# Kernel optimization log

Measured on AMD Instinct MI355X. Metric: run time of the kernel, lower is better.

The kernel has to match this reference:

```python
import jax, jax.numpy as jnp
import numpy as np

M, N, D, P = 1024, 1024, 64, 4096
H = N // D
L = P + M  # total KV length


def setup_inputs() -> dict:
    key = jax.random.key(0)
    ks = jax.random.split(key, 7)
    s = 1.0 / np.float32(np.sqrt(N))
    return {
        "X": jax.random.normal(ks[0], (M, N), jnp.float32),
        "W_q": jax.random.normal(ks[1], (N, N), jnp.float32) * s,
        "W_k": jax.random.normal(ks[2], (N, N), jnp.float32) * s,
        "W_v": jax.random.normal(ks[3], (N, N), jnp.float32) * s,
        "cache_K": jax.random.normal(ks[4], (H, P, D), jnp.float32),
        "cache_V": jax.random.normal(ks[5], (H, P, D), jnp.float32),
        "noise": jax.random.normal(ks[6], (H, M, L), jnp.float32) * 0.5,
    }


def reference(X, W_q, W_k, W_v, cache_K, cache_V, noise):
    # Projections: [M, N] -> [M, H, D]
    q = (X @ W_q).reshape(M, H, D)
    k = (X @ W_k).reshape(M, H, D).transpose(1, 0, 2)  # [H, M, D]
    v = (X @ W_v).reshape(M, H, D).transpose(1, 0, 2)  # [H, M, D]

    # KV cache concat (HND layout): [H, L, D]
    k_cache = jnp.concatenate([cache_K, k], axis=1)
    v_cache = jnp.concatenate([cache_V, v], axis=1)

    # Full QK^T scores, sm_scale=1.0, non-causal (flashinfer default): [H, M, L]
    scores = jnp.einsum("mhd,hld->hml", q, k_cache)
    weights = jax.nn.softmax(scores, axis=-1)  # == flash-attention probs (sm_scale=1.0)

    # Attention output: [M, H, D] -> [M, N]
    output = jnp.einsum("hml,hld->mhd", weights, v_cache).reshape(M, N)

    # Keyformer noise-perturbed importance softmax (temperature 1.5): [H, M, L]
    perturb_out = jax.nn.softmax((scores + noise) / 1.5, axis=-1)

    return output, weights, perturb_out
```

## Files before the change

kernel.cpp:

```cpp
#include <hip/hip_runtime.h>
#include <stdint.h>

#define MM 1024
#define NN 1024
#define DD 64
#define PP 4096
#define HH 16
#define LL 5120
#define SHC 12.0f

typedef float  f32x4  __attribute__((ext_vector_type(4)));
typedef short  s16x8  __attribute__((ext_vector_type(8)));
typedef short  s16x4  __attribute__((ext_vector_type(4)));
typedef __bf16 bf16x8 __attribute__((ext_vector_type(8)));

static __device__ __forceinline__ unsigned short f2bf(float f) {
    unsigned u = __float_as_uint(f);
    u += 0x7FFFu + ((u >> 16) & 1u);
    return (unsigned short)(u >> 16);
}
static __device__ __forceinline__ float bf2f(unsigned short h) {
    return __uint_as_float(((unsigned)h) << 16);
}
static __device__ __forceinline__ f32x4 mfma16(s16x8 a, s16x8 b, f32x4 c) {
    return __builtin_amdgcn_mfma_f32_16x16x32_bf16(
        __builtin_bit_cast(bf16x8, a), __builtin_bit_cast(bf16x8, b), c, 0, 0, 0);
}

__global__ void k_prep(const float* __restrict__ X, const float* __restrict__ cK,
                       unsigned short* __restrict__ Xh, unsigned short* __restrict__ Xl,
                       unsigned short* __restrict__ Kall) {
    const int nX4 = (MM * NN) / 4;
    const int nK4 = (HH * PP * DD) / 4;
    int stride = gridDim.x * blockDim.x;
    for (int i = blockIdx.x * blockDim.x + threadIdx.x; i < nX4 + nK4; i += stride) {
        if (i < nX4) {
            f32x4 v = reinterpret_cast<const f32x4*>(X)[i];
            s16x4 h, l;
            for (int j = 0; j < 4; ++j) {
                float f = v[j];
                unsigned short hb = f2bf(f);
                h[j] = (short)hb;
                l[j] = (short)f2bf(f - bf2f(hb));
            }
            reinterpret_cast<s16x4*>(Xh)[i] = h;
            reinterpret_cast<s16x4*>(Xl)[i] = l;
        } else {
            int j = i - nX4;
            f32x4 v = reinterpret_cast<const f32x4*>(cK)[j];
            s16x4 h;
            for (int jj = 0; jj < 4; ++jj) h[jj] = (short)f2bf(v[jj]);
            int e = j * 4;
            int hh = e >> 18;
            int rem = e & 262143;
            int64_t de = (int64_t)hh * (LL * DD) + rem;
            *reinterpret_cast<s16x4*>(Kall + de) = h;
        }
    }
}

__global__ void k_transW(const float* __restrict__ Wq, const float* __restrict__ Wk,
                         const float* __restrict__ Wv,
                         unsigned short* __restrict__ WhT, unsigned short* __restrict__ WlT) {
    __shared__ float t[64][68];
    int z = blockIdx.z;
    const float* W = (z == 0) ? Wq : ((z == 1) ? Wk : Wv);
    int n0 = blockIdx.x * 64, k0 = blockIdx.y * 64;
    int tc = threadIdx.x & 15, tr = threadIdx.x >> 4;
    for (int i = 0; i < 4; ++i) {
        int r = tr + i * 16;
        f32x4 v = *reinterpret_cast<const f32x4*>(W + (int64_t)(k0 + r) * NN + n0 + tc * 4);
        t[r][tc * 4 + 0] = v[0]; t[r][tc * 4 + 1] = v[1];
        t[r][tc * 4 + 2] = v[2]; t[r][tc * 4 + 3] = v[3];
    }
    __syncthreads();
    int64_t zoff = (int64_t)z * MM * NN;
    for (int i = 0; i < 4; ++i) {
        int rr = tr + i * 16;
        s16x4 h, l;
        for (int j = 0; j < 4; ++j) {
            float f = t[tc * 4 + j][rr];
            unsigned short hb = f2bf(f);
            h[j] = (short)hb;
            l[j] = (short)f2bf(f - bf2f(hb));
        }
        *reinterpret_cast<s16x4*>(WhT + zoff + (int64_t)(n0 + rr) * NN + k0 + tc * 4) = h;
        *reinterpret_cast<s16x4*>(WlT + zoff + (int64_t)(n0 + rr) * NN + k0 + tc * 4) = l;
    }
}

__launch_bounds__(256, 4)
__global__ void k_gemm(const unsigned short* __restrict__ Xh, const unsigned short* __restrict__ Xl,
                       const unsigned short* __restrict__ WhT, const unsigned short* __restrict__ WlT,
                       unsigned short* __restrict__ Qh, unsigned short* __restrict__ Ql,
                       unsigned short* __restrict__ Kall, unsigned short* __restrict__ Vproj) {
    __shared__ unsigned short sb[2 * 64 * 72];
    unsigned short* As = sb;
    unsigned short* Bs = sb + 64 * 72;
    int z = blockIdx.z;
    int n0 = blockIdx.x * 64, m0 = blockIdx.y * 64;
    int tid = threadIdx.x, lane = tid & 63, wave = tid >> 6;
    int lrow = lane & 15, lgrp = lane >> 4;
    int wm = (wave >> 1) * 32, wn = (wave & 1) * 32;
    f32x4 acc[2][2] = {};
    for (int seg = 0; seg < 3; ++seg) {
        const unsigned short* Asrc = (seg == 2) ? Xl : Xh;
        const unsigned short* Bsrc = ((seg == 1) ? WlT : WhT) + (int64_t)z * MM * NN;
        for (int kt = 0; kt < 16; ++kt) {
            int kb = kt * 64;
            for (int i = 0; i < 2; ++i) {
                int idx = i * 256 + tid;
                int r = idx >> 3, c8 = (idx & 7) * 8;
                *reinterpret_cast<s16x8*>(&As[r * 72 + c8]) =
                    *reinterpret_cast<const s16x8*>(Asrc + (int64_t)(m0 + r) * NN + kb + c8);
                *reinterpret_cast<s16x8*>(&Bs[r * 72 + c8]) =
                    *reinterpret_cast<const s16x8*>(Bsrc + (int64_t)(n0 + r) * NN + kb + c8);
            }
            __syncthreads();
            for (int ks = 0; ks < 2; ++ks) {
                s16x8 af[2], bfr[2];
                for (int f = 0; f < 2; ++f)
                    af[f] = *reinterpret_cast<const s16x8*>(&As[(wm + f * 16 + lrow) * 72 + ks * 32 + lgrp * 8]);
                for (int f = 0; f < 2; ++f)
                    bfr[f] = *reinterpret_cast<const s16x8*>(&Bs[(wn + f * 16 + lrow) * 72 + ks * 32 + lgrp * 8]);
                for (int i = 0; i < 2; ++i)
                    for (int j = 0; j < 2; ++j)
                        acc[i][j] = mfma16(af[i], bfr[j], acc[i][j]);
            }
            __syncthreads();
        }
    }
    unsigned short* Cs = sb;
    auto stageC = [&](int lo) {
        for (int i = 0; i < 2; ++i)
            for (int j = 0; j < 2; ++j)
                for (int r = 0; r < 4; ++r) {
                    float v = acc[i][j][r];
                    unsigned short hv = f2bf(v);
                    if (lo) hv = f2bf(v - bf2f(hv));
                    Cs[(wm + i * 16 + lgrp * 4 + r) * 72 + wn + j * 16 + lrow] = hv;
                }
    };
    auto writeC = [&](unsigned short* dst, int kmode) {
        for (int i = 0; i < 2; ++i) {
            int idx = i * 256 + tid;
            int r = idx >> 3, c8 = (idx & 7) * 8;
            s16x8 v = *reinterpret_cast<const s16x8*>(&Cs[r * 72 + c8]);
            int gm = m0 + r, gn = n0 + c8;
            if (kmode) {
                int hh = gn >> 6, d = gn & 63;
                *reinterpret_cast<s16x8*>(dst + ((int64_t)hh * LL + PP + gm) * DD + d) = v;
            } else {
                *reinterpret_cast<s16x8*>(dst + (int64_t)gm * NN + gn) = v;
            }
        }
    };
    __syncthreads();
    if (z == 0) {
        stageC(0); __syncthreads(); writeC(Qh, 0);
        __syncthreads(); stageC(1); __syncthreads(); writeC(Ql, 0);
    } else if (z == 1) {
        stageC(0); __syncthreads(); writeC(Kall, 1);
    } else {
        stageC(0); __syncthreads(); writeC(Vproj, 0);
    }
}

__global__ void k_transV(const float* __restrict__ cV, const unsigned short* __restrict__ Vproj,
                         unsigned short* __restrict__ VT) {
    __shared__ unsigned short Ts[64][72];
    int b = blockIdx.x;
    int hh = b / 80, lt = b % 80;
    int l0 = lt * 64;
    int tid = threadIdx.x;
    if (l0 < PP) {
        for (int i = 0; i < 4; ++i) {
            int idx = i * 256 + tid;
            int r = idx >> 4, c4 = (idx & 15) * 4;
            f32x4 v = *reinterpret_cast<const f32x4*>(cV + ((int64_t)hh * PP + l0 + r) * DD + c4);
            s16x4 o;
            for (int j = 0; j < 4; ++j) o[j] = (short)f2bf(v[j]);
            *reinterpret_cast<s16x4*>(&Ts[r][c4]) = o;
        }
    } else {
        for (int i = 0; i < 2; ++i) {
            int idx = i * 256 + tid;
            int r = idx >> 3, c8 = (idx & 7) * 8;
            *reinterpret_cast<s16x8*>(&Ts[r][c8]) =
                *reinterpret_cast<const s16x8*>(Vproj + (int64_t)(l0 - PP + r) * NN + hh * DD + c8);
        }
    }
    __syncthreads();
    for (int i = 0; i < 2; ++i) {
        int idx = i * 256 + tid;
        int d = idx >> 3, l8 = (idx & 7) * 8;
        s16x8 v;
        for (int j = 0; j < 8; ++j) v[j] = (short)Ts[l8 + j][d];
        *reinterpret_cast<s16x8*>(VT + ((int64_t)hh * DD + d) * LL + l0 + l8) = v;
    }
}

__launch_bounds__(256, 4)
__global__ void k_attn2(const unsigned short* __restrict__ Qh, const unsigned short* __restrict__ Ql,
                        const unsigned short* __restrict__ Kall, const unsigned short* __restrict__ VT,
                        const float* __restrict__ noise,
                        float* __restrict__ outO, float* __restrict__ outW, float* __restrict__ outP) {
    __shared__ __align__(16) char smem[26624];
    __shared__ float sred[4][16][2];
    __shared__ float siwp[16][2];

    int id = blockIdx.x;
    int xcd = id & 7, j = id >> 3;
    int hh = xcd * 2 + (j >> 6);
    int mt = j & 63;
    int m0 = mt * 16;
    int tid = threadIdx.x, lane = tid & 63, wave = tid >> 6;
    int lrow = lane & 15, lgrp = lane >> 4;

    float (*scf)[68] = (float(*)[68])(smem + wave * 6656);
    unsigned short (*wls)[72] = (unsigned short(*)[72])(smem + wave * 6656 + 4352);

    s16x8 aqh[2], aql[2];
    for (int ks = 0; ks < 2; ++ks) {
        int64_t off = (int64_t)(m0 + lrow) * NN + hh * DD + ks * 32 + lgrp * 8;
        aqh[ks] = *reinterpret_cast<const s16x8*>(Qh + off);
        aql[ks] = *reinterpret_cast<const s16x8*>(Ql + off);
    }
    const unsigned short* Kh = Kall + (int64_t)hh * LL * DD;
    const unsigned short* Vh = VT + (int64_t)hh * DD * LL;
    const float* nzw = noise + ((int64_t)hh * MM + m0) * LL;
    float* Wb = outW + ((int64_t)hh * MM + m0) * LL;
    float* Pb = outP + ((int64_t)hh * MM + m0) * LL;

    float SwR[4] = {}, SpR[4] = {};
    for (int c = 0; c < 20; ++c) {
        int lb = c * 256 + wave * 64;
        f32x4 nv[4];
        for (int rp = 0; rp < 4; ++rp)
            nv[rp] = *reinterpret_cast<const f32x4*>(
                nzw + (int64_t)(rp * 4 + lgrp) * LL + lb + lrow * 4);
        f32x4 sacc[4] = {};
        for (int ks = 0; ks < 2; ++ks)
            for (int lf = 0; lf < 4; ++lf) {
                s16x8 bk = *reinterpret_cast<const s16x8*>(
                    Kh + (int64_t)(lb + lf * 16 + lrow) * DD + ks * 32 + lgrp * 8);
                sacc[lf] = mfma16(aqh[ks], bk, sacc[lf]);
                sacc[lf] = mfma16(aql[ks], bk, sacc[lf]);
            }
        for (int lf = 0; lf < 4; ++lf)
            for (int r = 0; r < 4; ++r)
                scf[lgrp * 4 + r][lf * 16 + lrow] = sacc[lf][r];
        for (int rp = 0; rp < 4; ++rp) {
            f32x4 s = *reinterpret_cast<const f32x4*>(&scf[rp * 4 + lgrp][lrow * 4]);
            for (int jj = 0; jj < 4; ++jj) {
                SwR[rp] += __expf(s[jj] - SHC);
                SpR[rp] += __expf((s[jj] + nv[rp][jj]) * (1.f / 1.5f) - SHC);
            }
        }
    }
    for (int rp = 0; rp < 4; ++rp)
        for (int d = 1; d < 16; d <<= 1) {
            SwR[rp] += __shfl_xor(SwR[rp], d, 64);
            SpR[rp] += __shfl_xor(SpR[rp], d, 64);
        }
    if (lrow == 0)
        for (int rp = 0; rp < 4; ++rp) {
            sred[wave][rp * 4 + lgrp][0] = SwR[rp];
            sred[wave][rp * 4 + lgrp][1] = SpR[rp];
        }
    __syncthreads();
    if (tid < 32) {
        int row = tid >> 1, ty = tid & 1;
        float S = sred[0][row][ty] + sred[1][row][ty] + sred[2][row][ty] + sred[3][row][ty];
        siwp[row][ty] = 1.f / S;
    }
    __syncthreads();
    float iwr[4], ipr[4];
    for (int rp = 0; rp < 4; ++rp) {
        iwr[rp] = siwp[rp * 4 + lgrp][0];
        ipr[rp] = siwp[rp * 4 + lgrp][1];
    }

    f32x4 oacc[4] = {};
    for (int c = 19; c >= 0; --c) {
        int lb = c * 256 + wave * 64;
        f32x4 nv[4];
        for (int rp = 0; rp < 4; ++rp)
            nv[rp] = *reinterpret_cast<const f32x4*>(
                nzw + (int64_t)(rp * 4 + lgrp) * LL + lb + lrow * 4);
        f32x4 sacc[4] = {};
        for (int ks = 0; ks < 2; ++ks)
            for (int lf = 0; lf < 4; ++lf) {
                s16x8 bk = *reinterpret_cast<const s16x8*>(
                    Kh + (int64_t)(lb + lf * 16 + lrow) * DD + ks * 32 + lgrp * 8);
                sacc[lf] = mfma16(aqh[ks], bk, sacc[lf]);
                sacc[lf] = mfma16(aql[ks], bk, sacc[lf]);
            }
        for (int lf = 0; lf < 4; ++lf)
            for (int r = 0; r < 4; ++r)
                scf[lgrp * 4 + r][lf * 16 + lrow] = sacc[lf][r];
        for (int rp = 0; rp < 4; ++rp) {
            int row = rp * 4 + lgrp;
            f32x4 s = *reinterpret_cast<const f32x4*>(&scf[row][lrow * 4]);
            f32x4 wv, pv;
            for (int jj = 0; jj < 4; ++jj) {
                wv[jj] = __expf(s[jj] - SHC) * iwr[rp];
                pv[jj] = __expf((s[jj] + nv[rp][jj]) * (1.f / 1.5f) - SHC) * ipr[rp];
            }
            *reinterpret_cast<f32x4*>(Wb + (int64_t)row * LL + lb + lrow * 4) = wv;
            *reinterpret_cast<f32x4*>(Pb + (int64_t)row * LL + lb + lrow * 4) = pv;
            s16x4 pk;
            for (int jj = 0; jj < 4; ++jj) pk[jj] = (short)f2bf(wv[jj]);
            *reinterpret_cast<s16x4*>(&wls[row][lrow * 4]) = pk;
        }
        for (int ks = 0; ks < 2; ++ks) {
            s16x8 bw = *reinterpret_cast<const s16x8*>(&wls[lrow][ks * 32 + lgrp * 8]);
            for (int df = 0; df < 4; ++df) {
                s16x8 av = *reinterpret_cast<const s16x8*>(
                    Vh + (int64_t)(df * 16 + lrow) * LL + lb + ks * 32 + lgrp * 8);
                oacc[df] = mfma16(av, bw, oacc[df]);
            }
        }
    }
    __syncthreads();
    float* ored = (float*)smem;
    for (int df = 0; df < 4; ++df)
        for (int r = 0; r < 4; ++r)
            ored[(wave * 64 + df * 16 + lgrp * 4 + r) * 17 + lrow] = oacc[df][r];
    __syncthreads();
    for (int i = 0; i < 4; ++i) {
        int idx = i * 256 + tid;
        int m = idx >> 6, d = idx & 63;
        float v = ored[d * 17 + m] + ored[(64 + d) * 17 + m] +
                  ored[(128 + d) * 17 + m] + ored[(192 + d) * 17 + m];
        outO[(int64_t)(m0 + m) * NN + hh * DD + d] = v;
    }
}

extern "C" void kernel_launch(void* const* d_in, const int* in_sizes, int n_in,
                              void* d_out, int out_size, void* d_ws, size_t ws_size,
                              hipStream_t stream) {
    const float* X  = (const float*)d_in[0];
    const float* Wq = (const float*)d_in[1];
    const float* Wk = (const float*)d_in[2];
    const float* Wv = (const float*)d_in[3];
    const float* cK = (const float*)d_in[4];
    const float* cV = (const float*)d_in[5];
    const float* nz = (const float*)d_in[6];

    char* ws = (char*)d_ws;
    const int64_t U = 1 << 21;
    unsigned short* Xh    = (unsigned short*)(ws + 0 * U);
    unsigned short* Xl    = (unsigned short*)(ws + 1 * U);
    unsigned short* WhT   = (unsigned short*)(ws + 2 * U);
    unsigned short* WlT   = (unsigned short*)(ws + 5 * U);
    unsigned short* Qh    = (unsigned short*)(ws + 8 * U);
    unsigned short* Ql    = (unsigned short*)(ws + 9 * U);
    unsigned short* Kall  = (unsigned short*)(ws + 10 * U);
    unsigned short* Vproj = (unsigned short*)(ws + 15 * U);
    unsigned short* VT    = (unsigned short*)(ws + 16 * U);

    float* outO = (float*)d_out;
    float* outW = outO + (int64_t)MM * NN;
    float* outP = outW + (int64_t)HH * MM * LL;

    k_prep<<<2048, 256, 0, stream>>>(X, cK, Xh, Xl, Kall);
    k_transW<<<dim3(16, 16, 3), 256, 0, stream>>>(Wq, Wk, Wv, WhT, WlT);
    k_gemm<<<dim3(16, 16, 3), 256, 0, stream>>>(Xh, Xl, WhT, WlT, Qh, Ql, Kall, Vproj);
    k_transV<<<1280, 256, 0, stream>>>(cV, Vproj, VT);
    k_attn2<<<1024, 256, 0, stream>>>(Qh, Ql, Kall, VT, nz, outO, outW, outP);
}
```

Baseline: 513.6 us.

## Split attention into sum and emit kernels over KV halves with partial-output reduction

Splits the single two-pass attention kernel into a row-sum kernel and an emit kernel, each dividing the KV length into two halves, which doubles the grid to 2048 blocks. Partial softmax denominators and partial outputs go to workspace, and a small final kernel adds the two output halves. Noise is loaded per row inside the loop rather than prefetched, W/P stores become nontemporal, and the emit kernel walks blocks in reverse order, likely to reuse cached K and noise. The aim is more parallelism and occupancy. The cost is two extra launches, workspace traffic, and overwriting the Xh/WhT regions, which are no longer needed at that point.

```diff
diff --git a/kernel.cpp b/kernel.cpp
--- a/kernel.cpp
+++ b/kernel.cpp
@@ -200,25 +200,24 @@
     }
 }
 
-__launch_bounds__(256, 4)
-__global__ void k_attn2(const unsigned short* __restrict__ Qh, const unsigned short* __restrict__ Ql,
-                        const unsigned short* __restrict__ Kall, const unsigned short* __restrict__ VT,
-                        const float* __restrict__ noise,
-                        float* __restrict__ outO, float* __restrict__ outW, float* __restrict__ outP) {
-    __shared__ __align__(16) char smem[26624];
+__launch_bounds__(256, 8)
+__global__ void k_attnS(const unsigned short* __restrict__ Qh, const unsigned short* __restrict__ Ql,
+                        const unsigned short* __restrict__ Kall,
+                        const float* __restrict__ noise, float* __restrict__ wsS) {
+    __shared__ __align__(16) char smem[17408];
     __shared__ float sred[4][16][2];
-    __shared__ float siwp[16][2];
 
     int id = blockIdx.x;
-    int xcd = id & 7, j = id >> 3;
-    int hh = xcd * 2 + (j >> 6);
-    int mt = j & 63;
+    int xcd = id & 7, i = id >> 3;
+    int hh = xcd * 2 + (i >> 7);
+    int rem = i & 127;
+    int mt = rem >> 1, half = rem & 1;
     int m0 = mt * 16;
+    int w = hh * 128 + mt * 2 + half;
     int tid = threadIdx.x, lane = tid & 63, wave = tid >> 6;
     int lrow = lane & 15, lgrp = lane >> 4;
 
-    float (*scf)[68] = (float(*)[68])(smem + wave * 6656);
-    unsigned short (*wls)[72] = (unsigned short(*)[72])(smem + wave * 6656 + 4352);
+    float (*scf)[68] = (float(*)[68])(smem + wave * 4352);
 
     s16x8 aqh[2], aql[2];
     for (int ks = 0; ks < 2; ++ks) {
@@ -227,18 +226,11 @@
         aql[ks] = *reinterpret_cast<const s16x8*>(Ql + off);
     }
     const unsigned short* Kh = Kall + (int64_t)hh * LL * DD;
-    const unsigned short* Vh = VT + (int64_t)hh * DD * LL;
     const float* nzw = noise + ((int64_t)hh * MM + m0) * LL;
-    float* Wb = outW + ((int64_t)hh * MM + m0) * LL;
-    float* Pb = outP + ((int64_t)hh * MM + m0) * LL;
 
     float SwR[4] = {}, SpR[4] = {};
-    for (int c = 0; c < 20; ++c) {
-        int lb = c * 256 + wave * 64;
-        f32x4 nv[4];
-        for (int rp = 0; rp < 4; ++rp)
-            nv[rp] = *reinterpret_cast<const f32x4*>(
-                nzw + (int64_t)(rp * 4 + lgrp) * LL + lb + lrow * 4);
+    for (int c = 0; c < 10; ++c) {
+        int lb = half * 2560 + c * 256 + wave * 64;
         f32x4 sacc[4] = {};
         for (int ks = 0; ks < 2; ++ks)
             for (int lf = 0; lf < 4; ++lf) {
@@ -251,10 +243,12 @@
             for (int r = 0; r < 4; ++r)
                 scf[lgrp * 4 + r][lf * 16 + lrow] = sacc[lf][r];
         for (int rp = 0; rp < 4; ++rp) {
-            f32x4 s = *reinterpret_cast<const f32x4*>(&scf[rp * 4 + lgrp][lrow * 4]);
+            int row = rp * 4 + lgrp;
+            f32x4 s = *reinterpret_cast<const f32x4*>(&scf[row][lrow * 4]);
+            f32x4 nv = *reinterpret_cast<const f32x4*>(nzw + (int64_t)row * LL + lb + lrow * 4);
             for (int jj = 0; jj < 4; ++jj) {
                 SwR[rp] += __expf(s[jj] - SHC);
-                SpR[rp] += __expf((s[jj] + nv[rp][jj]) * (1.f / 1.5f) - SHC);
+                SpR[rp] += __expf((s[jj] + nv[jj]) * (1.f / 1.5f) - SHC);
             }
         }
     }
@@ -271,23 +265,55 @@
     __syncthreads();
     if (tid < 32) {
         int row = tid >> 1, ty = tid & 1;
-        float S = sred[0][row][ty] + sred[1][row][ty] + sred[2][row][ty] + sred[3][row][ty];
-        siwp[row][ty] = 1.f / S;
-    }
-    __syncthreads();
+        wsS[w * 32 + tid] = sred[0][row][ty] + sred[1][row][ty] +
+                            sred[2][row][ty] + sred[3][row][ty];
+    }
+}
+
+__launch_bounds__(256, 6)
+__global__ void k_attnE(const unsigned short* __restrict__ Qh, const unsigned short* __restrict__ Ql,
+                        const unsigned short* __restrict__ Kall, const unsigned short* __restrict__ VT,
+                        const float* __restrict__ noise, const float* __restrict__ wsS,
+                        float* __restrict__ wsO, float* __restrict__ outW, float* __restrict__ outP) {
+    __shared__ __align__(16) char smem[17408];
+
+    int id = blockIdx.x;
+    int xcd = id & 7, i = 255 - (id >> 3);
+    int hh = xcd * 2 + (i >> 7);
+    int rem = i & 127;
+    int mt = rem >> 1, half = rem & 1;
+    int m0 = mt * 16;
+    int w = hh * 128 + mt * 2 + half;
+    int tid = threadIdx.x, lane = tid & 63, wave = tid >> 6;
+    int lrow = lane & 15, lgrp = lane >> 4;
+
+    float (*scf)[68] = (float(*)[68])(smem + wave * 4352);
+    unsigned short* wl = (unsigned short*)scf;
+
+    s16x8 aqh[2], aql[2];
+    for (int ks = 0; ks < 2; ++ks) {
+        int64_t off = (int64_t)(m0 + lrow) * NN + hh * DD + ks * 32 + lgrp * 8;
+        aqh[ks] = *reinterpret_cast<const s16x8*>(Qh + off);
+        aql[ks] = *reinterpret_cast<const s16x8*>(Ql + off);
+    }
+    const unsigned short* Kh = Kall + (int64_t)hh * LL * DD;
+    const unsigned short* Vh = VT + (int64_t)hh * DD * LL;
+    const float* nzw = noise + ((int64_t)hh * MM + m0) * LL;
+    float* Wb = outW + ((int64_t)hh * MM + m0) * LL;
+    float* Pb = outP + ((int64_t)hh * MM + m0) * LL;
+
     float iwr[4], ipr[4];
     for (int rp = 0; rp < 4; ++rp) {
-        iwr[rp] = siwp[rp * 4 + lgrp][0];
-        ipr[rp] = siwp[rp * 4 + lgrp][1];
+        int row = rp * 4 + lgrp;
+        float sw = wsS[w * 32 + row * 2]     + wsS[(w ^ 1) * 32 + row * 2];
+        float sp = wsS[w * 32 + row * 2 + 1] + wsS[(w ^ 1) * 32 + row * 2 + 1];
+        iwr[rp] = 1.f / sw;
+        ipr[rp] = 1.f / sp;
     }
 
     f32x4 oacc[4] = {};
-    for (int c = 19; c >= 0; --c) {
-        int lb = c * 256 + wave * 64;
-        f32x4 nv[4];
-        for (int rp = 0; rp < 4; ++rp)
-            nv[rp] = *reinterpret_cast<const f32x4*>(
-                nzw + (int64_t)(rp * 4 + lgrp) * LL + lb + lrow * 4);
+    for (int c = 9; c >= 0; --c) {
+        int lb = half * 2560 + c * 256 + wave * 64;
         f32x4 sacc[4] = {};
         for (int ks = 0; ks < 2; ++ks)
             for (int lf = 0; lf < 4; ++lf) {
@@ -302,19 +328,20 @@
         for (int rp = 0; rp < 4; ++rp) {
             int row = rp * 4 + lgrp;
             f32x4 s = *reinterpret_cast<const f32x4*>(&scf[row][lrow * 4]);
+            f32x4 nv = *reinterpret_cast<const f32x4*>(nzw + (int64_t)row * LL + lb + lrow * 4);
             f32x4 wv, pv;
             for (int jj = 0; jj < 4; ++jj) {
                 wv[jj] = __expf(s[jj] - SHC) * iwr[rp];
-                pv[jj] = __expf((s[jj] + nv[rp][jj]) * (1.f / 1.5f) - SHC) * ipr[rp];
-            }
-            *reinterpret_cast<f32x4*>(Wb + (int64_t)row * LL + lb + lrow * 4) = wv;
-            *reinterpret_cast<f32x4*>(Pb + (int64_t)row * LL + lb + lrow * 4) = pv;
+                pv[jj] = __expf((s[jj] + nv[jj]) * (1.f / 1.5f) - SHC) * ipr[rp];
+            }
+            __builtin_nontemporal_store(wv, reinterpret_cast<f32x4*>(Wb + (int64_t)row * LL + lb + lrow * 4));
+            __builtin_nontemporal_store(pv, reinterpret_cast<f32x4*>(Pb + (int64_t)row * LL + lb + lrow * 4));
             s16x4 pk;
             for (int jj = 0; jj < 4; ++jj) pk[jj] = (short)f2bf(wv[jj]);
-            *reinterpret_cast<s16x4*>(&wls[row][lrow * 4]) = pk;
+            *reinterpret_cast<s16x4*>(&wl[row * 136 + lrow * 4]) = pk;
         }
         for (int ks = 0; ks < 2; ++ks) {
-            s16x8 bw = *reinterpret_cast<const s16x8*>(&wls[lrow][ks * 32 + lgrp * 8]);
+            s16x8 bw = *reinterpret_cast<const s16x8*>(&wl[lrow * 136 + ks * 32 + lgrp * 8]);
             for (int df = 0; df < 4; ++df) {
                 s16x8 av = *reinterpret_cast<const s16x8*>(
                     Vh + (int64_t)(df * 16 + lrow) * LL + lb + ks * 32 + lgrp * 8);
@@ -328,12 +355,25 @@
         for (int r = 0; r < 4; ++r)
             ored[(wave * 64 + df * 16 + lgrp * 4 + r) * 17 + lrow] = oacc[df][r];
     __syncthreads();
-    for (int i = 0; i < 4; ++i) {
-        int idx = i * 256 + tid;
-        int m = idx >> 6, d = idx & 63;
+    for (int i2 = 0; i2 < 4; ++i2) {
+        int e = i2 * 256 + tid;
+        int m = e >> 6, d = e & 63;
         float v = ored[d * 17 + m] + ored[(64 + d) * 17 + m] +
                   ored[(128 + d) * 17 + m] + ored[(192 + d) * 17 + m];
-        outO[(int64_t)(m0 + m) * NN + hh * DD + d] = v;
+        wsO[(int64_t)w * 1024 + m * 64 + d] = v;
+    }
+}
+
+__global__ void k_ofin(const float* __restrict__ wsO, float* __restrict__ outO) {
+    int bid = blockIdx.x;
+    int hh = bid >> 6, mt = bid & 63;
+    int w0 = bid * 2;
+    int tid = threadIdx.x;
+    for (int i = 0; i < 4; ++i) {
+        int e = i * 256 + tid;
+        int m = e >> 6, d = e & 63;
+        float v = wsO[(int64_t)w0 * 1024 + e] + wsO[(int64_t)(w0 + 1) * 1024 + e];
+        __builtin_nontemporal_store(v, outO + (int64_t)(mt * 16 + m) * NN + hh * DD + d);
     }
 }
 
@@ -359,6 +399,8 @@
     unsigned short* Kall  = (unsigned short*)(ws + 10 * U);
     unsigned short* Vproj = (unsigned short*)(ws + 15 * U);
     unsigned short* VT    = (unsigned short*)(ws + 16 * U);
+    float* wsO = (float*)(ws + 0 * U);
+    float* wsS = (float*)(ws + 4 * U);
 
     float* outO = (float*)d_out;
     float* outW = outO + (int64_t)MM * NN;
@@ -368,5 +410,7 @@
     k_transW<<<dim3(16, 16, 3), 256, 0, stream>>>(Wq, Wk, Wv, WhT, WlT);
     k_gemm<<<dim3(16, 16, 3), 256, 0, stream>>>(Xh, Xl, WhT, WlT, Qh, Ql, Kall, Vproj);
     k_transV<<<1280, 256, 0, stream>>>(cV, Vproj, VT);
-    k_attn2<<<1024, 256, 0, stream>>>(Qh, Ql, Kall, VT, nz, outO, outW, outP);
-}
+    k_attnS<<<2048, 256, 0, stream>>>(Qh, Ql, Kall, nz, wsS);
+    k_attnE<<<2048, 256, 0, stream>>>(Qh, Ql, Kall, VT, nz, wsS, wsO, outW, outP);
+    k_ofin<<<1024, 256, 0, stream>>>(wsO, outO);
+}
```

Measured after the change: 630.1 us. 22.7% more time.
